# Kernel optimization log

Measured on AMD Instinct MI355X. Metric: run time of the kernel, lower is better.

## Reference

```python
import jax, jax.numpy as jnp
import numpy as np

B, S, E, NUM_CLASSES = 4, 4096, 256, 16

def setup_inputs() -> dict:
    key = jax.random.key(0)
    ks = jax.random.split(key, 10)
    std = E ** -0.5
    return {
        "x":  jax.random.normal(ks[0], (B, S, E), dtype=jnp.float32),
        "wq": jax.random.normal(ks[1], (E, E), dtype=jnp.float32) * std,
        "bq": jnp.zeros((E,), dtype=jnp.float32),
        "wk": jax.random.normal(ks[2], (E, E), dtype=jnp.float32) * std,
        "bk": jnp.zeros((E,), dtype=jnp.float32),
        "wv": jax.random.normal(ks[3], (E, E), dtype=jnp.float32) * std,
        "bv": jnp.zeros((E,), dtype=jnp.float32),
        "wo": jax.random.normal(ks[4], (NUM_CLASSES, E), dtype=jnp.float32) * std,
        "bo": jnp.zeros((NUM_CLASSES,), dtype=jnp.float32),
    }

def reference(x, wq, bq, wk, bk, wv, bv, wo, bo):
    embed_dim = wq.shape[0]
    scaling = embed_dim ** -0.5  # float(embed_dim) ** (-0.5)
    # torch Linear: y = x @ W.T + b
    Q = jnp.einsum('bse,oe->bso', x, wq) + bq
    K = jnp.einsum('bse,oe->bso', x, wk) + bk
    V = jnp.einsum('bse,oe->bso', x, wv) + bv
    # scores: [B, S, S]
    scores = jnp.einsum('bqe,bke->bqk', Q, K) * scaling
    # original code has `/ (embed_dim ^ 0.5)`; intended math is / sqrt(embed_dim)
    attn = jax.nn.softmax(scores, axis=-1) * scaling
    attn_out = jnp.einsum('bqk,bke->bqe', attn, V)
    return jnp.einsum('bqe,oe->bqo', attn_out, wo) + bo
```

## Files before the change

kernel.cpp:

```cpp
#include <hip/hip_runtime.h>
#include <hip/hip_bf16.h>


#define S_ 4096
#define E_ 256
#define B_ 4
#define NC_ 16
#define BS_ (B_ * S_)
#define NS_ 4

typedef __attribute__((ext_vector_type(8))) short bf16x8;
typedef __attribute__((ext_vector_type(4))) float f32x4;

__device__ __forceinline__ unsigned short bf16_rtne(float f) {
    unsigned int u = __float_as_uint(f);
    return (unsigned short)((u + 0x7FFFu + ((u >> 16) & 1u)) >> 16);
}
__device__ __forceinline__ bf16x8 pack8(f32x4 a, f32x4 b) {
    bf16x8 r;
#pragma unroll
    for (int i = 0; i < 4; i++) r[i] = (short)bf16_rtne(a[i]);
#pragma unroll
    for (int i = 0; i < 4; i++) r[4 + i] = (short)bf16_rtne(b[i]);
    return r;
}
__device__ __forceinline__ void gl_lds16(const void* g, void* lds) {
    __builtin_amdgcn_global_load_lds(
        (const __attribute__((address_space(1))) unsigned int*)g,
        (__attribute__((address_space(3))) unsigned int*)lds, 16, 0, 0);
}
__device__ __forceinline__ int swz_u(int q) { return q ^ ((q >> 3) & 7); }

__global__ __launch_bounds__(256) void qkv_gemm(
    const float* __restrict__ x, const float* __restrict__ wq,
    const float* __restrict__ wk, const float* __restrict__ wv,
    const float* __restrict__ bq, const float* __restrict__ bk,
    const float* __restrict__ bv, short* __restrict__ Qb,
    short* __restrict__ Kb, short* __restrict__ Vtc,
    float* __restrict__ partial) {
    __shared__ __align__(16) short stg[2][8192];
    __shared__ __align__(16) short epi[16896];

    int t = threadIdx.x;
    int lin = blockIdx.x;
    int xcd = lin & 7, r8 = lin >> 3;
    int sel = r8 >> 5;
    int m0 = (((xcd << 5) | (r8 & 31))) * 64;
    int lane = t & 63, wid = t >> 6, quad = lane >> 4, idx = lane & 15;

    const float* wsel = (sel == 0) ? wq : (sel == 1) ? wk : wv;
    const float* bias = (sel == 0) ? bq : (sel == 1) ? bk : bv;

    const float* wsrc[4];
#pragma unroll
    for (int i = 0; i < 4; i++) {
        int q = i * 256 + t, u = swz_u(q);
        wsrc[i] = wsel + (size_t)(u >> 2) * E_ + (u & 3) * 8;
    }

    f32x4 wf[8];
#pragma unroll
    for (int i = 0; i < 4; i++) {
        wf[i * 2] = *(const f32x4*)(wsrc[i]);
        wf[i * 2 + 1] = *(const f32x4*)(wsrc[i] + 4);
    }

    {
        int z = lin * 256 + t;
        partial[z] = 0.f;
        if (z < BS_ * NC_ - 196608) partial[z + 196608] = 0.f;
    }

    const float* xrow = x + (size_t)(m0 + wid * 16 + idx) * E_ + quad * 8;
    bf16x8 af[8];
#pragma unroll
    for (int it = 0; it < 8; it++) {
        f32x4 a0 = *(const f32x4*)(xrow + it * 32);
        f32x4 a1 = *(const f32x4*)(xrow + it * 32 + 4);
        af[it] = pack8(a0, a1);
    }

#pragma unroll
    for (int i = 0; i < 4; i++)
        *(bf16x8*)&stg[0][(i * 256 + t) * 8] = pack8(wf[i * 2], wf[i * 2 + 1]);

    f32x4 zf = {0.f, 0.f, 0.f, 0.f};
    f32x4 acc[16];
#pragma unroll
    for (int i = 0; i < 16; i++) acc[i] = zf;

    int fo = (idx * 4 + quad) ^ (idx >> 1);

    __syncthreads();

#pragma unroll
    for (int it = 0; it < 8; it++) {
        if (it < 7) {
            int kc = (it + 1) * 32;
#pragma unroll
            for (int i = 0; i < 4; i++) {
                wf[i * 2] = *(const f32x4*)(wsrc[i] + kc);
                wf[i * 2 + 1] = *(const f32x4*)(wsrc[i] + kc + 4);
            }
        }
        const short* cw = &stg[it & 1][fo * 8];
        __builtin_amdgcn_s_setprio(1);
#pragma unroll
        for (int ct = 0; ct < 16; ct++)
            acc[ct] = __builtin_amdgcn_mfma_f32_16x16x32_bf16(
                af[it], *(const bf16x8*)&cw[ct * 512], acc[ct], 0, 0, 0);
        __builtin_amdgcn_s_setprio(0);
        if (it < 7) {
            short* d = stg[(it + 1) & 1];
#pragma unroll
            for (int i = 0; i < 4; i++)
                *(bf16x8*)&d[(i * 256 + t) * 8] = pack8(wf[i * 2], wf[i * 2 + 1]);
        }
        __syncthreads();
    }

    int qr = quad * 4;
    if (sel == 2) {
#pragma unroll
        for (int ct = 0; ct < 16; ct++) {
            int e = ct * 16 + idx;
            float bb = bias[e];
#pragma unroll
            for (int r = 0; r < 4; r++) {
                int mr = wid * 16 + qr + r;
                int ckg = mr >> 5, sin = mr & 31;
                int sp = ((sin & 15) << 1) | (sin >> 4);
                int pos = (sp >> 3) ^ ((e >> 1) & 3);
                epi[ckg * 8192 + e * 32 + pos * 8 + (sp & 7)] =
                    (short)bf16_rtne(acc[ct][r] + bb);
            }
        }
        __syncthreads();
        size_t base = ((size_t)((m0 >> 12) * 128 + ((m0 & (S_ - 1)) >> 5))) * 8192;
#pragma unroll
        for (int j = 0; j < 8; j++) {
            int unit = j * 256 + t;
            *(bf16x8*)(Vtc + base + (size_t)unit * 8) = *(const bf16x8*)&epi[unit * 8];
        }
    } else {
        float alpha = (sel == 0) ? 0.0625f : 1.0f;
#pragma unroll
        for (int ct = 0; ct < 16; ct++) {
            int n = ct * 16 + idx;
            float bb = bias[n];
#pragma unroll
            for (int r = 0; r < 4; r++) {
                int row = wid * 16 + qr + r;
                int col = (sel == 1) ? ((((n >> 3) ^ (row & 7)) << 3) | (n & 7)) : n;
                epi[row * 264 + col] = (short)bf16_rtne((acc[ct][r] + bb) * alpha);
            }
        }
        __syncthreads();
        short* out = (sel == 0) ? Qb : Kb;
#pragma unroll
        for (int j = 0; j < 8; j++) {
            int g = j * 256 + t;
            int row = g >> 5, seg = g & 31;
            *(bf16x8*)(out + (size_t)(m0 + row) * E_ + seg * 8) =
                *(const bf16x8*)&epi[row * 264 + seg * 8];
        }
    }
}

__global__ __launch_bounds__(256, 2) void flash_attn(
    const short* __restrict__ Qb, const short* __restrict__ Kb,
    const short* __restrict__ Vtc, const float* __restrict__ wo,
    float* __restrict__ partial, float* __restrict__ lpart) {
    __shared__ __align__(16) short lds[37888];

    int t = threadIdx.x;
    int lin = blockIdx.x;
    int xcd = lin & 7, r8 = lin >> 3;
    int pair = (xcd << 1) | (r8 >> 5);
    int b = pair >> 2, slice = pair & 3, q0 = (r8 & 31) * 128;
    int key0 = slice * (S_ / NS_);
    const int nchunk = (S_ / NS_) / 32;
    int lane = t & 63, wv = t >> 6, quad = lane >> 4, idx = lane & 15;

    bf16x8 qf[2][8];
#pragma unroll
    for (int u = 0; u < 2; u++) {
        const short* qrow = Qb + (size_t)(b * S_ + q0 + u * 64 + wv * 16 + idx) * E_ + quad * 8;
#pragma unroll
        for (int c = 0; c < 8; c++) qf[u][c] = *(const bf16x8*)(qrow + c * 32);
    }

    f32x4 zf = {0.f, 0.f, 0.f, 0.f};
    f32x4 oacc[2][16];
#pragma unroll
    for (int u = 0; u < 2; u++)
#pragma unroll
        for (int i = 0; i < 16; i++) oacc[u][i] = zf;
    float ls[2][4] = {{0, 0, 0, 0}, {0, 0, 0, 0}};

    const short* kg = Kb + (size_t)(b * S_ + key0) * E_ + lane * 8;
    const short* vg = Vtc + ((size_t)(b * 128 + (key0 >> 5))) * 8192 + lane * 8;
    short* psw = lds + 32768 + wv * 1280;
    unsigned int* pswu = (unsigned int*)psw;
    int vsw = (quad ^ ((idx >> 1) & 3)) << 3;

#pragma unroll
    for (int j = 0; j < 4; j++) gl_lds16(kg + (wv * 4 + j) * 512, &lds[(wv * 4 + j) * 512]);
#pragma unroll
    for (int j = 0; j < 4; j++) gl_lds16(vg + (wv * 4 + j) * 512, &lds[16384 + (wv * 4 + j) * 512]);
#pragma unroll
    for (int j = 0; j < 4; j++) gl_lds16(kg + 8192 + (wv * 4 + j) * 512, &lds[8192 + (wv * 4 + j) * 512]);
    __syncthreads();

    {
        f32x4 s[4] = {zf, zf, zf, zf};
        __builtin_amdgcn_s_setprio(1);
#pragma unroll
        for (int c = 0; c < 8; c++) {
            int p = (((c * 4 + quad) ^ (idx & 7)) << 3);
            bf16x8 k0 = *(const bf16x8*)&lds[idx * 256 + p];
            bf16x8 k1 = *(const bf16x8*)&lds[(16 + idx) * 256 + p];
            s[0] = __builtin_amdgcn_mfma_f32_16x16x32_bf16(qf[0][c], k0, s[0], 0, 0, 0);
            s[1] = __builtin_amdgcn_mfma_f32_16x16x32_bf16(qf[0][c], k1, s[1], 0, 0, 0);
            s[2] = __builtin_amdgcn_mfma_f32_16x16x32_bf16(qf[1][c], k0, s[2], 0, 0, 0);
            s[3] = __builtin_amdgcn_mfma_f32_16x16x32_bf16(qf[1][c], k1, s[3], 0, 0, 0);
        }
        __builtin_amdgcn_s_setprio(0);
#pragma unroll
        for (int u = 0; u < 2; u++)
#pragma unroll
            for (int r = 0; r < 4; r++) {
                float p0 = __expf(s[u * 2][r]);
                float p1 = __expf(s[u * 2 + 1][r]);
                ls[u][r] += p0 + p1;
                pswu[u * 320 + (quad * 4 + r) * 20 + idx] =
                    (unsigned int)bf16_rtne(p0) | ((unsigned int)bf16_rtne(p1) << 16);
            }
    }

    for (int ck = 0; ck < nchunk - 1; ck++) {
        __syncthreads();
        bf16x8 af0 = *(const bf16x8*)&psw[idx * 40 + quad * 8];
        bf16x8 af1 = *(const bf16x8*)&psw[640 + idx * 40 + quad * 8];
        if (ck + 2 < nchunk) {
            const short* ks = kg + (size_t)(ck + 2) * 8192;
            short* kd = lds + (ck & 1) * 8192;
#pragma unroll
            for (int j = 0; j < 4; j++) gl_lds16(ks + (wv * 4 + j) * 512, &kd[(wv * 4 + j) * 512]);
        }
        {
            const short* vs = vg + (size_t)(ck + 1) * 8192;
            short* vd = lds + 16384 + ((ck + 1) & 1) * 8192;
#pragma unroll
            for (int j = 0; j < 4; j++) gl_lds16(vs + (wv * 4 + j) * 512, &vd[(wv * 4 + j) * 512]);
        }
        const short* kc = lds + ((ck + 1) & 1) * 8192;
        f32x4 s[4] = {zf, zf, zf, zf};
        __builtin_amdgcn_s_setprio(1);
#pragma unroll
        for (int c = 0; c < 8; c++) {
            int p = (((c * 4 + quad) ^ (idx & 7)) << 3);
            bf16x8 k0 = *(const bf16x8*)&kc[idx * 256 + p];
            bf16x8 k1 = *(const bf16x8*)&kc[(16 + idx) * 256 + p];
            s[0] = __builtin_amdgcn_mfma_f32_16x16x32_bf16(qf[0][c], k0, s[0], 0, 0, 0);
            s[1] = __builtin_amdgcn_mfma_f32_16x16x32_bf16(qf[0][c], k1, s[1], 0, 0, 0);
            s[2] = __builtin_amdgcn_mfma_f32_16x16x32_bf16(qf[1][c], k0, s[2], 0, 0, 0);
            s[3] = __builtin_amdgcn_mfma_f32_16x16x32_bf16(qf[1][c], k1, s[3], 0, 0, 0);
        }
        __builtin_amdgcn_s_setprio(0);
#pragma unroll
        for (int u = 0; u < 2; u++)
#pragma unroll
            for (int r = 0; r < 4; r++) {
                float p0 = __expf(s[u * 2][r]);
                float p1 = __expf(s[u * 2 + 1][r]);
                ls[u][r] += p0 + p1;
                pswu[u * 320 + (quad * 4 + r) * 20 + idx] =
                    (unsigned int)bf16_rtne(p0) | ((unsigned int)bf16_rtne(p1) << 16);
            }
        const short* vc = lds + 16384 + (ck & 1) * 8192;
        __builtin_amdgcn_s_setprio(1);
#pragma unroll
        for (int ct = 0; ct < 16; ct++) {
            bf16x8 v = *(const bf16x8*)&vc[(ct * 16 + idx) * 32 + vsw];
            oacc[0][ct] = __builtin_amdgcn_mfma_f32_16x16x32_bf16(af0, v, oacc[0][ct], 0, 0, 0);
            oacc[1][ct] = __builtin_amdgcn_mfma_f32_16x16x32_bf16(af1, v, oacc[1][ct], 0, 0, 0);
        }
        __builtin_amdgcn_s_setprio(0);
    }
    __syncthreads();
    {
        bf16x8 af0 = *(const bf16x8*)&psw[idx * 40 + quad * 8];
        bf16x8 af1 = *(const bf16x8*)&psw[640 + idx * 40 + quad * 8];
        const short* vc = lds + 16384 + ((nchunk - 1) & 1) * 8192;
        __builtin_amdgcn_s_setprio(1);
#pragma unroll
        for (int ct = 0; ct < 16; ct++) {
            bf16x8 v = *(const bf16x8*)&vc[(ct * 16 + idx) * 32 + vsw];
            oacc[0][ct] = __builtin_amdgcn_mfma_f32_16x16x32_bf16(af0, v, oacc[0][ct], 0, 0, 0);
            oacc[1][ct] = __builtin_amdgcn_mfma_f32_16x16x32_bf16(af1, v, oacc[1][ct], 0, 0, 0);
        }
        __builtin_amdgcn_s_setprio(0);
    }
    __syncthreads();

#pragma unroll
    for (int u = 0; u < 2; u++)
#pragma unroll
        for (int r = 0; r < 4; r++) {
            float v = ls[u][r];
            v += __shfl_xor(v, 1);
            v += __shfl_xor(v, 2);
            v += __shfl_xor(v, 4);
            v += __shfl_xor(v, 8);
            if (idx == 0)
                lpart[(size_t)slice * BS_ + b * S_ + q0 + u * 64 + wv * 16 + quad * 4 + r] = v;
        }

    short* scr = lds + wv * 8192;
#pragma unroll
    for (int u = 0; u < 2; u++)
#pragma unroll
        for (int ct = 0; ct < 16; ct++) {
            int e = ct * 16 + idx;
#pragma unroll
            for (int r = 0; r < 4; r++) {
                int lr = quad * 4 + r;
                scr[u * 4096 + lr * 256 + ((((e >> 3) ^ (lr & 7)) << 3) | (e & 7))] =
                    (short)bf16_rtne(oacc[u][ct][r]);
            }
        }

    f32x4 pacc[2] = {zf, zf};
#pragma unroll
    for (int c = 0; c < 8; c++) {
        const float* ws = wo + idx * E_ + c * 32 + quad * 8;
        bf16x8 bw = pack8(*(const f32x4*)ws, *(const f32x4*)(ws + 4));
#pragma unroll
        for (int u = 0; u < 2; u++) {
            bf16x8 pa = *(const bf16x8*)&scr[u * 4096 + idx * 256 +
                                             (((c * 4 + quad) ^ (idx & 7)) << 3)];
            pacc[u] = __builtin_amdgcn_mfma_f32_16x16x32_bf16(pa, bw, pacc[u], 0, 0, 0);
        }
    }
#pragma unroll
    for (int u = 0; u < 2; u++)
#pragma unroll
        for (int r = 0; r < 4; r++) {
            int m = q0 + u * 64 + wv * 16 + quad * 4 + r;
            atomicAdd(&partial[((size_t)b * S_ + m) * NC_ + idx], pacc[u][r]);
        }
}

__global__ __launch_bounds__(256) void norm_out(
    const float* __restrict__ partial, const float* __restrict__ lpart,
    const float* __restrict__ bo, float* __restrict__ out) {
    int t = threadIdx.x;
    int m = blockIdx.x * 16 + (t >> 4), o = t & 15;
    float ltot = 0.f;
#pragma unroll
    for (int ns = 0; ns < NS_; ns++) ltot += lpart[(size_t)ns * BS_ + m];
    size_t i = (size_t)m * NC_ + o;
    out[i] = partial[i] * (0.0625f / ltot) + bo[o];
}

extern "C" void kernel_launch(void* const* d_in, const int* in_sizes, int n_in,
                              void* d_out, int out_size, void* d_ws, size_t ws_size,
                              hipStream_t stream) {
    const float* x  = (const float*)d_in[0];
    const float* wq = (const float*)d_in[1];
    const float* bq = (const float*)d_in[2];
    const float* wk = (const float*)d_in[3];
    const float* bk = (const float*)d_in[4];
    const float* wv = (const float*)d_in[5];
    const float* bv = (const float*)d_in[6];
    const float* wo = (const float*)d_in[7];
    const float* bo = (const float*)d_in[8];
    float* out = (float*)d_out;

    const size_t NEL = (size_t)BS_ * E_;
    short* Qb = (short*)d_ws;
    short* Kb = Qb + NEL;
    short* Vtc = Kb + NEL;
    float* partial = (float*)(Vtc + NEL);
    float* lpart = partial + (size_t)BS_ * NC_;

    qkv_gemm<<<dim3(768), 256, 0, stream>>>(x, wq, wk, wv, bq, bk, bv, Qb, Kb, Vtc, partial);
    flash_attn<<<dim3(512), 256, 0, stream>>>(Qb, Kb, Vtc, wo, partial, lpart);
    norm_out<<<dim3(BS_ / 16), 256, 0, stream>>>(partial, lpart, bo, out);
}
```

Before: 172.6 us.

## Fuse QKV GEMM, attention, and normalization into one persistent kernel with grid barriers

Merges the three kernels into one launch of 512 blocks. The 768 QKV tiles are spread over two passes, and software grid-wide barriers built on atomic counters separate the QKV, attention and output-normalization phases. This removes two kernel launch gaps and the separate norm kernel. In exchange it adds a hipMemsetAsync for the barrier counters, atomic spin-wait barriers, and a tail where only half the blocks run the second QKV pass. It also relies on all 512 blocks being co-resident (2 per CU), or the barrier deadlocks.

```diff
diff --git a/kernel.cpp b/kernel.cpp
--- a/kernel.cpp
+++ b/kernel.cpp
@@ -31,337 +31,342 @@
 }
 __device__ __forceinline__ int swz_u(int q) { return q ^ ((q >> 3) & 7); }
 
-__global__ __launch_bounds__(256) void qkv_gemm(
+__device__ __forceinline__ void gbar(unsigned* ctr, unsigned nblk) {
+    __threadfence();
+    __syncthreads();
+    if (threadIdx.x == 0) {
+        atomicAdd(ctr, 1u);
+        while (atomicAdd(ctr, 0u) < nblk) __builtin_amdgcn_s_sleep(2);
+    }
+    __syncthreads();
+    __threadfence();
+}
+
+__global__ __launch_bounds__(256, 2) void fused(
     const float* __restrict__ x, const float* __restrict__ wq,
     const float* __restrict__ wk, const float* __restrict__ wv,
     const float* __restrict__ bq, const float* __restrict__ bk,
-    const float* __restrict__ bv, short* __restrict__ Qb,
+    const float* __restrict__ bv, const float* __restrict__ wo,
+    const float* __restrict__ bo, short* __restrict__ Qb,
     short* __restrict__ Kb, short* __restrict__ Vtc,
-    float* __restrict__ partial) {
-    __shared__ __align__(16) short stg[2][8192];
-    __shared__ __align__(16) short epi[16896];
-
+    float* __restrict__ partial, float* __restrict__ lpart,
+    unsigned* __restrict__ bars, float* __restrict__ out) {
+    __shared__ __align__(16) short lds[37888];
     int t = threadIdx.x;
-    int lin = blockIdx.x;
-    int xcd = lin & 7, r8 = lin >> 3;
-    int sel = r8 >> 5;
-    int m0 = (((xcd << 5) | (r8 & 31))) * 64;
+    int bid = blockIdx.x;
     int lane = t & 63, wid = t >> 6, quad = lane >> 4, idx = lane & 15;
-
-    const float* wsel = (sel == 0) ? wq : (sel == 1) ? wk : wv;
-    const float* bias = (sel == 0) ? bq : (sel == 1) ? bk : bv;
-
-    const float* wsrc[4];
-#pragma unroll
-    for (int i = 0; i < 4; i++) {
-        int q = i * 256 + t, u = swz_u(q);
-        wsrc[i] = wsel + (size_t)(u >> 2) * E_ + (u & 3) * 8;
-    }
-
-    f32x4 wf[8];
-#pragma unroll
-    for (int i = 0; i < 4; i++) {
-        wf[i * 2] = *(const f32x4*)(wsrc[i]);
-        wf[i * 2 + 1] = *(const f32x4*)(wsrc[i] + 4);
-    }
+    f32x4 zf = {0.f, 0.f, 0.f, 0.f};
 
     {
-        int z = lin * 256 + t;
+        int z = bid * 256 + t;
         partial[z] = 0.f;
-        if (z < BS_ * NC_ - 196608) partial[z + 196608] = 0.f;
-    }
-
-    const float* xrow = x + (size_t)(m0 + wid * 16 + idx) * E_ + quad * 8;
-    bf16x8 af[8];
-#pragma unroll
-    for (int it = 0; it < 8; it++) {
-        f32x4 a0 = *(const f32x4*)(xrow + it * 32);
-        f32x4 a1 = *(const f32x4*)(xrow + it * 32 + 4);
-        af[it] = pack8(a0, a1);
-    }
-
-#pragma unroll
-    for (int i = 0; i < 4; i++)
-        *(bf16x8*)&stg[0][(i * 256 + t) * 8] = pack8(wf[i * 2], wf[i * 2 + 1]);
-
-    f32x4 zf = {0.f, 0.f, 0.f, 0.f};
-    f32x4 acc[16];
-#pragma unroll
-    for (int i = 0; i < 16; i++) acc[i] = zf;
-
-    int fo = (idx * 4 + quad) ^ (idx >> 1);
-
-    __syncthreads();
-
-#pragma unroll
-    for (int it = 0; it < 8; it++) {
-        if (it < 7) {
-            int kc = (it + 1) * 32;
-#pragma unroll
-            for (int i = 0; i < 4; i++) {
-                wf[i * 2] = *(const f32x4*)(wsrc[i] + kc);
-                wf[i * 2 + 1] = *(const f32x4*)(wsrc[i] + kc + 4);
-            }
-        }
-        const short* cw = &stg[it & 1][fo * 8];
-        __builtin_amdgcn_s_setprio(1);
-#pragma unroll
-        for (int ct = 0; ct < 16; ct++)
-            acc[ct] = __builtin_amdgcn_mfma_f32_16x16x32_bf16(
-                af[it], *(const bf16x8*)&cw[ct * 512], acc[ct], 0, 0, 0);
-        __builtin_amdgcn_s_setprio(0);
-        if (it < 7) {
-            short* d = stg[(it + 1) & 1];
-#pragma unroll
-            for (int i = 0; i < 4; i++)
-                *(bf16x8*)&d[(i * 256 + t) * 8] = pack8(wf[i * 2], wf[i * 2 + 1]);
-        }
-        __syncthreads();
-    }
-
-    int qr = quad * 4;
-    if (sel == 2) {
-#pragma unroll
-        for (int ct = 0; ct < 16; ct++) {
-            int e = ct * 16 + idx;
-            float bb = bias[e];
+        partial[z + 131072] = 0.f;
+    }
+    for (int pass = 0; pass < 2; ++pass) {
+        if (pass == 1 && bid >= 256) break;
+        int lin = bid + pass * 512;
+        int xcd = lin & 7, r8 = lin >> 3;
+        int sel = r8 >> 5;
+        int m0 = (((xcd << 5) | (r8 & 31))) * 64;
+
+        const float* wsel = (sel == 0) ? wq : (sel == 1) ? wk : wv;
+        const float* bias = (sel == 0) ? bq : (sel == 1) ? bk : bv;
+        short* ep = lds + 16384;
+
+        const float* wsrc[4];
+#pragma unroll
+        for (int i = 0; i < 4; i++) {
+            int q = i * 256 + t, u = swz_u(q);
+            wsrc[i] = wsel + (size_t)(u >> 2) * E_ + (u & 3) * 8;
+        }
+        f32x4 wf[8];
+#pragma unroll
+        for (int i = 0; i < 4; i++) {
+            wf[i * 2] = *(const f32x4*)(wsrc[i]);
+            wf[i * 2 + 1] = *(const f32x4*)(wsrc[i] + 4);
+        }
+        const float* xrow = x + (size_t)(m0 + wid * 16 + idx) * E_ + quad * 8;
+        bf16x8 af[8];
+#pragma unroll
+        for (int it = 0; it < 8; it++) {
+            f32x4 a0 = *(const f32x4*)(xrow + it * 32);
+            f32x4 a1 = *(const f32x4*)(xrow + it * 32 + 4);
+            af[it] = pack8(a0, a1);
+        }
+#pragma unroll
+        for (int i = 0; i < 4; i++)
+            *(bf16x8*)&lds[(i * 256 + t) * 8] = pack8(wf[i * 2], wf[i * 2 + 1]);
+
+        f32x4 acc[16];
+#pragma unroll
+        for (int i = 0; i < 16; i++) acc[i] = zf;
+        int fo = (idx * 4 + quad) ^ (idx >> 1);
+
+        __syncthreads();
+#pragma unroll
+        for (int it = 0; it < 8; it++) {
+            if (it < 7) {
+                int kc = (it + 1) * 32;
+#pragma unroll
+                for (int i = 0; i < 4; i++) {
+                    wf[i * 2] = *(const f32x4*)(wsrc[i] + kc);
+                    wf[i * 2 + 1] = *(const f32x4*)(wsrc[i] + kc + 4);
+                }
+            }
+            const short* cw = &lds[((it & 1) * 1024 + fo) * 8];
+            __builtin_amdgcn_s_setprio(1);
+#pragma unroll
+            for (int ct = 0; ct < 16; ct++)
+                acc[ct] = __builtin_amdgcn_mfma_f32_16x16x32_bf16(
+                    af[it], *(const bf16x8*)&cw[ct * 512], acc[ct], 0, 0, 0);
+            __builtin_amdgcn_s_setprio(0);
+            if (it < 7) {
+                short* d = lds + ((it + 1) & 1) * 8192;
+#pragma unroll
+                for (int i = 0; i < 4; i++)
+                    *(bf16x8*)&d[(i * 256 + t) * 8] = pack8(wf[i * 2], wf[i * 2 + 1]);
+            }
+            __syncthreads();
+        }
+
+        int qr = quad * 4;
+        if (sel == 2) {
+#pragma unroll
+            for (int ct = 0; ct < 16; ct++) {
+                int e = ct * 16 + idx;
+                float bb = bias[e];
+#pragma unroll
+                for (int r = 0; r < 4; r++) {
+                    int mr = wid * 16 + qr + r;
+                    int ckg = mr >> 5, sin = mr & 31;
+                    int sp = ((sin & 15) << 1) | (sin >> 4);
+                    int pos = (sp >> 3) ^ ((e >> 1) & 3);
+                    ep[ckg * 8192 + e * 32 + pos * 8 + (sp & 7)] =
+                        (short)bf16_rtne(acc[ct][r] + bb);
+                }
+            }
+            __syncthreads();
+            size_t base = ((size_t)((m0 >> 12) * 128 + ((m0 & (S_ - 1)) >> 5))) * 8192;
+#pragma unroll
+            for (int j = 0; j < 8; j++) {
+                int unit = j * 256 + t;
+                *(bf16x8*)(Vtc + base + (size_t)unit * 8) = *(const bf16x8*)&ep[unit * 8];
+            }
+        } else {
+            float alpha = (sel == 0) ? 0.0625f : 1.0f;
+#pragma unroll
+            for (int ct = 0; ct < 16; ct++) {
+                int n = ct * 16 + idx;
+                float bb = bias[n];
+#pragma unroll
+                for (int r = 0; r < 4; r++) {
+                    int row = wid * 16 + qr + r;
+                    int col = (sel == 1) ? ((((n >> 3) ^ (row & 7)) << 3) | (n & 7)) : n;
+                    ep[row * 264 + col] = (short)bf16_rtne((acc[ct][r] + bb) * alpha);
+                }
+            }
+            __syncthreads();
+            short* o = (sel == 0) ? Qb : Kb;
+#pragma unroll
+            for (int j = 0; j < 8; j++) {
+                int g = j * 256 + t;
+                int row = g >> 5, seg = g & 31;
+                *(bf16x8*)(o + (size_t)(m0 + row) * E_ + seg * 8) =
+                    *(const bf16x8*)&ep[row * 264 + seg * 8];
+            }
+        }
+        __syncthreads();
+    }
+
+    gbar(&bars[0], 512);
+
+    {
+        int lin = bid;
+        int xcd = lin & 7, r8 = lin >> 3;
+        int pair = (xcd << 1) | (r8 >> 5);
+        int b = pair >> 2, slice = pair & 3, q0 = (r8 & 31) * 128;
+        int key0 = slice * (S_ / NS_);
+        const int nchunk = (S_ / NS_) / 32;
+        int wv = wid;
+
+        bf16x8 qf[2][8];
+#pragma unroll
+        for (int u = 0; u < 2; u++) {
+            const short* qrow = Qb + (size_t)(b * S_ + q0 + u * 64 + wv * 16 + idx) * E_ + quad * 8;
+#pragma unroll
+            for (int c = 0; c < 8; c++) qf[u][c] = *(const bf16x8*)(qrow + c * 32);
+        }
+        f32x4 oacc[2][16];
+#pragma unroll
+        for (int u = 0; u < 2; u++)
+#pragma unroll
+            for (int i = 0; i < 16; i++) oacc[u][i] = zf;
+        float ls[2][4] = {{0, 0, 0, 0}, {0, 0, 0, 0}};
+
+        const short* kg = Kb + (size_t)(b * S_ + key0) * E_ + lane * 8;
+        const short* vg = Vtc + ((size_t)(b * 128 + (key0 >> 5))) * 8192 + lane * 8;
+        short* psw = lds + 32768 + wv * 1280;
+        unsigned int* pswu = (unsigned int*)psw;
+        int vsw = (quad ^ ((idx >> 1) & 3)) << 3;
+
+#pragma unroll
+        for (int j = 0; j < 4; j++) gl_lds16(kg + (wv * 4 + j) * 512, &lds[(wv * 4 + j) * 512]);
+#pragma unroll
+        for (int j = 0; j < 4; j++) gl_lds16(vg + (wv * 4 + j) * 512, &lds[16384 + (wv * 4 + j) * 512]);
+#pragma unroll
+        for (int j = 0; j < 4; j++) gl_lds16(kg + 8192 + (wv * 4 + j) * 512, &lds[8192 + (wv * 4 + j) * 512]);
+        __syncthreads();
+
+        {
+            f32x4 s[4] = {zf, zf, zf, zf};
+            __builtin_amdgcn_s_setprio(1);
+#pragma unroll
+            for (int c = 0; c < 8; c++) {
+                int p = (((c * 4 + quad) ^ (idx & 7)) << 3);
+                bf16x8 k0 = *(const bf16x8*)&lds[idx * 256 + p];
+                bf16x8 k1 = *(const bf16x8*)&lds[(16 + idx) * 256 + p];
+                s[0] = __builtin_amdgcn_mfma_f32_16x16x32_bf16(qf[0][c], k0, s[0], 0, 0, 0);
+                s[1] = __builtin_amdgcn_mfma_f32_16x16x32_bf16(qf[0][c], k1, s[1], 0, 0, 0);
+                s[2] = __builtin_amdgcn_mfma_f32_16x16x32_bf16(qf[1][c], k0, s[2], 0, 0, 0);
+                s[3] = __builtin_amdgcn_mfma_f32_16x16x32_bf16(qf[1][c], k1, s[3], 0, 0, 0);
+            }
+            __builtin_amdgcn_s_setprio(0);
+#pragma unroll
+            for (int u = 0; u < 2; u++)
+#pragma unroll
+                for (int r = 0; r < 4; r++) {
+                    float p0 = __expf(s[u * 2][r]);
+                    float p1 = __expf(s[u * 2 + 1][r]);
+                    ls[u][r] += p0 + p1;
+                    pswu[u * 320 + (quad * 4 + r) * 20 + idx] =
+                        (unsigned int)bf16_rtne(p0) | ((unsigned int)bf16_rtne(p1) << 16);
+                }
+        }
+
+        for (int ck = 0; ck < nchunk - 1; ck++) {
+            __syncthreads();
+            bf16x8 af0 = *(const bf16x8*)&psw[idx * 40 + quad * 8];
+            bf16x8 af1 = *(const bf16x8*)&psw[640 + idx * 40 + quad * 8];
+            if (ck + 2 < nchunk) {
+                const short* ks = kg + (size_t)(ck + 2) * 8192;
+                short* kd = lds + (ck & 1) * 8192;
+#pragma unroll
+                for (int j = 0; j < 4; j++) gl_lds16(ks + (wv * 4 + j) * 512, &kd[(wv * 4 + j) * 512]);
+            }
+            {
+                const short* vs = vg + (size_t)(ck + 1) * 8192;
+                short* vd = lds + 16384 + ((ck + 1) & 1) * 8192;
+#pragma unroll
+                for (int j = 0; j < 4; j++) gl_lds16(vs + (wv * 4 + j) * 512, &vd[(wv * 4 + j) * 512]);
+            }
+            const short* kc = lds + ((ck + 1) & 1) * 8192;
+            f32x4 s[4] = {zf, zf, zf, zf};
+            __builtin_amdgcn_s_setprio(1);
+#pragma unroll
+            for (int c = 0; c < 8; c++) {
+                int p = (((c * 4 + quad) ^ (idx & 7)) << 3);
+                bf16x8 k0 = *(const bf16x8*)&kc[idx * 256 + p];
+                bf16x8 k1 = *(const bf16x8*)&kc[(16 + idx) * 256 + p];
+                s[0] = __builtin_amdgcn_mfma_f32_16x16x32_bf16(qf[0][c], k0, s[0], 0, 0, 0);
+                s[1] = __builtin_amdgcn_mfma_f32_16x16x32_bf16(qf[0][c], k1, s[1], 0, 0, 0);
+                s[2] = __builtin_amdgcn_mfma_f32_16x16x32_bf16(qf[1][c], k0, s[2], 0, 0, 0);
+                s[3] = __builtin_amdgcn_mfma_f32_16x16x32_bf16(qf[1][c], k1, s[3], 0, 0, 0);
+            }
+            __builtin_amdgcn_s_setprio(0);
+#pragma unroll
+            for (int u = 0; u < 2; u++)
+#pragma unroll
+                for (int r = 0; r < 4; r++) {
+                    float p0 = __expf(s[u * 2][r]);
+                    float p1 = __expf(s[u * 2 + 1][r]);
+                    ls[u][r] += p0 + p1;
+                    pswu[u * 320 + (quad * 4 + r) * 20 + idx] =
+                        (unsigned int)bf16_rtne(p0) | ((unsigned int)bf16_rtne(p1) << 16);
+                }
+            const short* vc = lds + 16384 + (ck & 1) * 8192;
+            __builtin_amdgcn_s_setprio(1);
+#pragma unroll
+            for (int ct = 0; ct < 16; ct++) {
+                bf16x8 v = *(const bf16x8*)&vc[(ct * 16 + idx) * 32 + vsw];
+                oacc[0][ct] = __builtin_amdgcn_mfma_f32_16x16x32_bf16(af0, v, oacc[0][ct], 0, 0, 0);
+                oacc[1][ct] = __builtin_amdgcn_mfma_f32_16x16x32_bf16(af1, v, oacc[1][ct], 0, 0, 0);
+            }
+            __builtin_amdgcn_s_setprio(0);
+        }
+        __syncthreads();
+        {
+            bf16x8 af0 = *(const bf16x8*)&psw[idx * 40 + quad * 8];
+            bf16x8 af1 = *(const bf16x8*)&psw[640 + idx * 40 + quad * 8];
+            const short* vc = lds + 16384 + ((nchunk - 1) & 1) * 8192;
+            __builtin_amdgcn_s_setprio(1);
+#pragma unroll
+            for (int ct = 0; ct < 16; ct++) {
+                bf16x8 v = *(const bf16x8*)&vc[(ct * 16 + idx) * 32 + vsw];
+                oacc[0][ct] = __builtin_amdgcn_mfma_f32_16x16x32_bf16(af0, v, oacc[0][ct], 0, 0, 0);
+                oacc[1][ct] = __builtin_amdgcn_mfma_f32_16x16x32_bf16(af1, v, oacc[1][ct], 0, 0, 0);
+            }
+            __builtin_amdgcn_s_setprio(0);
+        }
+        __syncthreads();
+
+#pragma unroll
+        for (int u = 0; u < 2; u++)
 #pragma unroll
             for (int r = 0; r < 4; r++) {
-                int mr = wid * 16 + qr + r;
-                int ckg = mr >> 5, sin = mr & 31;
-                int sp = ((sin & 15) << 1) | (sin >> 4);
-                int pos = (sp >> 3) ^ ((e >> 1) & 3);
-                epi[ckg * 8192 + e * 32 + pos * 8 + (sp & 7)] =
-                    (short)bf16_rtne(acc[ct][r] + bb);
-            }
-        }
-        __syncthreads();
-        size_t base = ((size_t)((m0 >> 12) * 128 + ((m0 & (S_ - 1)) >> 5))) * 8192;
-#pragma unroll
-        for (int j = 0; j < 8; j++) {
-            int unit = j * 256 + t;
-            *(bf16x8*)(Vtc + base + (size_t)unit * 8) = *(const bf16x8*)&epi[unit * 8];
-        }
-    } else {
-        float alpha = (sel == 0) ? 0.0625f : 1.0f;
-#pragma unroll
-        for (int ct = 0; ct < 16; ct++) {
-            int n = ct * 16 + idx;
-            float bb = bias[n];
+                float v = ls[u][r];
+                v += __shfl_xor(v, 1);
+                v += __shfl_xor(v, 2);
+                v += __shfl_xor(v, 4);
+                v += __shfl_xor(v, 8);
+                if (idx == 0)
+                    lpart[(size_t)slice * BS_ + b * S_ + q0 + u * 64 + wv * 16 + quad * 4 + r] = v;
+            }
+
+        short* scr = lds + wv * 8192;
+#pragma unroll
+        for (int u = 0; u < 2; u++)
+#pragma unroll
+            for (int ct = 0; ct < 16; ct++) {
+                int e = ct * 16 + idx;
+#pragma unroll
+                for (int r = 0; r < 4; r++) {
+                    int lr = quad * 4 + r;
+                    scr[u * 4096 + lr * 256 + ((((e >> 3) ^ (lr & 7)) << 3) | (e & 7))] =
+                        (short)bf16_rtne(oacc[u][ct][r]);
+                }
+            }
+        f32x4 pacc[2] = {zf, zf};
+#pragma unroll
+        for (int c = 0; c < 8; c++) {
+            const float* ws = wo + idx * E_ + c * 32 + quad * 8;
+            bf16x8 bw = pack8(*(const f32x4*)ws, *(const f32x4*)(ws + 4));
+#pragma unroll
+            for (int u = 0; u < 2; u++) {
+                bf16x8 pa = *(const bf16x8*)&scr[u * 4096 + idx * 256 +
+                                                 (((c * 4 + quad) ^ (idx & 7)) << 3)];
+                pacc[u] = __builtin_amdgcn_mfma_f32_16x16x32_bf16(pa, bw, pacc[u], 0, 0, 0);
+            }
+        }
+#pragma unroll
+        for (int u = 0; u < 2; u++)
 #pragma unroll
             for (int r = 0; r < 4; r++) {
-                int row = wid * 16 + qr + r;
-                int col = (sel == 1) ? ((((n >> 3) ^ (row & 7)) << 3) | (n & 7)) : n;
-                epi[row * 264 + col] = (short)bf16_rtne((acc[ct][r] + bb) * alpha);
-            }
-        }
-        __syncthreads();
-        short* out = (sel == 0) ? Qb : Kb;
-#pragma unroll
-        for (int j = 0; j < 8; j++) {
-            int g = j * 256 + t;
-            int row = g >> 5, seg = g & 31;
-            *(bf16x8*)(out + (size_t)(m0 + row) * E_ + seg * 8) =
-                *(const bf16x8*)&epi[row * 264 + seg * 8];
-        }
-    }
-}
-
-__global__ __launch_bounds__(256, 2) void flash_attn(
-    const short* __restrict__ Qb, const short* __restrict__ Kb,
-    const short* __restrict__ Vtc, const float* __restrict__ wo,
-    float* __restrict__ partial, float* __restrict__ lpart) {
-    __shared__ __align__(16) short lds[37888];
-
-    int t = threadIdx.x;
-    int lin = blockIdx.x;
-    int xcd = lin & 7, r8 = lin >> 3;
-    int pair = (xcd << 1) | (r8 >> 5);
-    int b = pair >> 2, slice = pair & 3, q0 = (r8 & 31) * 128;
-    int key0 = slice * (S_ / NS_);
-    const int nchunk = (S_ / NS_) / 32;
-    int lane = t & 63, wv = t >> 6, quad = lane >> 4, idx = lane & 15;
-
-    bf16x8 qf[2][8];
-#pragma unroll
-    for (int u = 0; u < 2; u++) {
-        const short* qrow = Qb + (size_t)(b * S_ + q0 + u * 64 + wv * 16 + idx) * E_ + quad * 8;
-#pragma unroll
-        for (int c = 0; c < 8; c++) qf[u][c] = *(const bf16x8*)(qrow + c * 32);
-    }
-
-    f32x4 zf = {0.f, 0.f, 0.f, 0.f};
-    f32x4 oacc[2][16];
-#pragma unroll
-    for (int u = 0; u < 2; u++)
-#pragma unroll
-        for (int i = 0; i < 16; i++) oacc[u][i] = zf;
-    float ls[2][4] = {{0, 0, 0, 0}, {0, 0, 0, 0}};
-
-    const short* kg = Kb + (size_t)(b * S_ + key0) * E_ + lane * 8;
-    const short* vg = Vtc + ((size_t)(b * 128 + (key0 >> 5))) * 8192 + lane * 8;
-    short* psw = lds + 32768 + wv * 1280;
-    unsigned int* pswu = (unsigned int*)psw;
-    int vsw = (quad ^ ((idx >> 1) & 3)) << 3;
-
-#pragma unroll
-    for (int j = 0; j < 4; j++) gl_lds16(kg + (wv * 4 + j) * 512, &lds[(wv * 4 + j) * 512]);
-#pragma unroll
-    for (int j = 0; j < 4; j++) gl_lds16(vg + (wv * 4 + j) * 512, &lds[16384 + (wv * 4 + j) * 512]);
-#pragma unroll
-    for (int j = 0; j < 4; j++) gl_lds16(kg + 8192 + (wv * 4 + j) * 512, &lds[8192 + (wv * 4 + j) * 512]);
-    __syncthreads();
-
-    {
-        f32x4 s[4] = {zf, zf, zf, zf};
-        __builtin_amdgcn_s_setprio(1);
-#pragma unroll
-        for (int c = 0; c < 8; c++) {
-            int p = (((c * 4 + quad) ^ (idx & 7)) << 3);
-            bf16x8 k0 = *(const bf16x8*)&lds[idx * 256 + p];
-            bf16x8 k1 = *(const bf16x8*)&lds[(16 + idx) * 256 + p];
-            s[0] = __builtin_amdgcn_mfma_f32_16x16x32_bf16(qf[0][c], k0, s[0], 0, 0, 0);
-            s[1] = __builtin_amdgcn_mfma_f32_16x16x32_bf16(qf[0][c], k1, s[1], 0, 0, 0);
-            s[2] = __builtin_amdgcn_mfma_f32_16x16x32_bf16(qf[1][c], k0, s[2], 0, 0, 0);
-            s[3] = __builtin_amdgcn_mfma_f32_16x16x32_bf16(qf[1][c], k1, s[3], 0, 0, 0);
-        }
-        __builtin_amdgcn_s_setprio(0);
-#pragma unroll
-        for (int u = 0; u < 2; u++)
-#pragma unroll
-            for (int r = 0; r < 4; r++) {
-                float p0 = __expf(s[u * 2][r]);
-                float p1 = __expf(s[u * 2 + 1][r]);
-                ls[u][r] += p0 + p1;
-                pswu[u * 320 + (quad * 4 + r) * 20 + idx] =
-                    (unsigned int)bf16_rtne(p0) | ((unsigned int)bf16_rtne(p1) << 16);
-            }
-    }
-
-    for (int ck = 0; ck < nchunk - 1; ck++) {
-        __syncthreads();
-        bf16x8 af0 = *(const bf16x8*)&psw[idx * 40 + quad * 8];
-        bf16x8 af1 = *(const bf16x8*)&psw[640 + idx * 40 + quad * 8];
-        if (ck + 2 < nchunk) {
-            const short* ks = kg + (size_t)(ck + 2) * 8192;
-            short* kd = lds + (ck & 1) * 8192;
-#pragma unroll
-            for (int j = 0; j < 4; j++) gl_lds16(ks + (wv * 4 + j) * 512, &kd[(wv * 4 + j) * 512]);
-        }
-        {
-            const short* vs = vg + (size_t)(ck + 1) * 8192;
-            short* vd = lds + 16384 + ((ck + 1) & 1) * 8192;
-#pragma unroll
-            for (int j = 0; j < 4; j++) gl_lds16(vs + (wv * 4 + j) * 512, &vd[(wv * 4 + j) * 512]);
-        }
-        const short* kc = lds + ((ck + 1) & 1) * 8192;
-        f32x4 s[4] = {zf, zf, zf, zf};
-        __builtin_amdgcn_s_setprio(1);
-#pragma unroll
-        for (int c = 0; c < 8; c++) {
-            int p = (((c * 4 + quad) ^ (idx & 7)) << 3);
-            bf16x8 k0 = *(const bf16x8*)&kc[idx * 256 + p];
-            bf16x8 k1 = *(const bf16x8*)&kc[(16 + idx) * 256 + p];
-            s[0] = __builtin_amdgcn_mfma_f32_16x16x32_bf16(qf[0][c], k0, s[0], 0, 0, 0);
-            s[1] = __builtin_amdgcn_mfma_f32_16x16x32_bf16(qf[0][c], k1, s[1], 0, 0, 0);
-            s[2] = __builtin_amdgcn_mfma_f32_16x16x32_bf16(qf[1][c], k0, s[2], 0, 0, 0);
-            s[3] = __builtin_amdgcn_mfma_f32_16x16x32_bf16(qf[1][c], k1, s[3], 0, 0, 0);
-        }
-        __builtin_amdgcn_s_setprio(0);
-#pragma unroll
-        for (int u = 0; u < 2; u++)
-#pragma unroll
-            for (int r = 0; r < 4; r++) {
-                float p0 = __expf(s[u * 2][r]);
-                float p1 = __expf(s[u * 2 + 1][r]);
-                ls[u][r] += p0 + p1;
-                pswu[u * 320 + (quad * 4 + r) * 20 + idx] =
-                    (unsigned int)bf16_rtne(p0) | ((unsigned int)bf16_rtne(p1) << 16);
-            }
-        const short* vc = lds + 16384 + (ck & 1) * 8192;
-        __builtin_amdgcn_s_setprio(1);
-#pragma unroll
-        for (int ct = 0; ct < 16; ct++) {
-            bf16x8 v = *(const bf16x8*)&vc[(ct * 16 + idx) * 32 + vsw];
-            oacc[0][ct] = __builtin_amdgcn_mfma_f32_16x16x32_bf16(af0, v, oacc[0][ct], 0, 0, 0);
-            oacc[1][ct] = __builtin_amdgcn_mfma_f32_16x16x32_bf16(af1, v, oacc[1][ct], 0, 0, 0);
-        }
-        __builtin_amdgcn_s_setprio(0);
-    }
-    __syncthreads();
-    {
-        bf16x8 af0 = *(const bf16x8*)&psw[idx * 40 + quad * 8];
-        bf16x8 af1 = *(const bf16x8*)&psw[640 + idx * 40 + quad * 8];
-        const short* vc = lds + 16384 + ((nchunk - 1) & 1) * 8192;
-        __builtin_amdgcn_s_setprio(1);
-#pragma unroll
-        for (int ct = 0; ct < 16; ct++) {
-            bf16x8 v = *(const bf16x8*)&vc[(ct * 16 + idx) * 32 + vsw];
-            oacc[0][ct] = __builtin_amdgcn_mfma_f32_16x16x32_bf16(af0, v, oacc[0][ct], 0, 0, 0);
-            oacc[1][ct] = __builtin_amdgcn_mfma_f32_16x16x32_bf16(af1, v, oacc[1][ct], 0, 0, 0);
-        }
-        __builtin_amdgcn_s_setprio(0);
-    }
-    __syncthreads();
-
-#pragma unroll
-    for (int u = 0; u < 2; u++)
-#pragma unroll
-        for (int r = 0; r < 4; r++) {
-            float v = ls[u][r];
-            v += __shfl_xor(v, 1);
-            v += __shfl_xor(v, 2);
-            v += __shfl_xor(v, 4);
-            v += __shfl_xor(v, 8);
-            if (idx == 0)
-                lpart[(size_t)slice * BS_ + b * S_ + q0 + u * 64 + wv * 16 + quad * 4 + r] = v;
-        }
-
-    short* scr = lds + wv * 8192;
-#pragma unroll
-    for (int u = 0; u < 2; u++)
-#pragma unroll
-        for (int ct = 0; ct < 16; ct++) {
-            int e = ct * 16 + idx;
-#pragma unroll
-            for (int r = 0; r < 4; r++) {
-                int lr = quad * 4 + r;
-                scr[u * 4096 + lr * 256 + ((((e >> 3) ^ (lr & 7)) << 3) | (e & 7))] =
-                    (short)bf16_rtne(oacc[u][ct][r]);
-            }
-        }
-
-    f32x4 pacc[2] = {zf, zf};
-#pragma unroll
-    for (int c = 0; c < 8; c++) {
-        const float* ws = wo + idx * E_ + c * 32 + quad * 8;
-        bf16x8 bw = pack8(*(const f32x4*)ws, *(const f32x4*)(ws + 4));
-#pragma unroll
-        for (int u = 0; u < 2; u++) {
-            bf16x8 pa = *(const bf16x8*)&scr[u * 4096 + idx * 256 +
-                                             (((c * 4 + quad) ^ (idx & 7)) << 3)];
-            pacc[u] = __builtin_amdgcn_mfma_f32_16x16x32_bf16(pa, bw, pacc[u], 0, 0, 0);
-        }
-    }
-#pragma unroll
-    for (int u = 0; u < 2; u++)
-#pragma unroll
-        for (int r = 0; r < 4; r++) {
-            int m = q0 + u * 64 + wv * 16 + quad * 4 + r;
-            atomicAdd(&partial[((size_t)b * S_ + m) * NC_ + idx], pacc[u][r]);
-        }
-}
-
-__global__ __launch_bounds__(256) void norm_out(
-    const float* __restrict__ partial, const float* __restrict__ lpart,
-    const float* __restrict__ bo, float* __restrict__ out) {
-    int t = threadIdx.x;
-    int m = blockIdx.x * 16 + (t >> 4), o = t & 15;
-    float ltot = 0.f;
-#pragma unroll
-    for (int ns = 0; ns < NS_; ns++) ltot += lpart[(size_t)ns * BS_ + m];
-    size_t i = (size_t)m * NC_ + o;
-    out[i] = partial[i] * (0.0625f / ltot) + bo[o];
+                int m = q0 + u * 64 + wv * 16 + quad * 4 + r;
+                atomicAdd(&partial[((size_t)b * S_ + m) * NC_ + idx], pacc[u][r]);
+            }
+    }
+
+    gbar(&bars[1], 512);
+
+#pragma unroll
+    for (int k = 0; k < 2; k++) {
+        int e = bid * 512 + k * 256 + t;
+        int m = e >> 4, o = e & 15;
+        float ltot = 0.f;
+#pragma unroll
+        for (int ns = 0; ns < NS_; ns++) ltot += lpart[(size_t)ns * BS_ + m];
+        out[e] = partial[e] * (0.0625f / ltot) + bo[o];
+    }
 }
 
 extern "C" void kernel_launch(void* const* d_in, const int* in_sizes, int n_in,
@@ -384,8 +389,9 @@
     short* Vtc = Kb + NEL;
     float* partial = (float*)(Vtc + NEL);
     float* lpart = partial + (size_t)BS_ * NC_;
-
-    qkv_gemm<<<dim3(768), 256, 0, stream>>>(x, wq, wk, wv, bq, bk, bv, Qb, Kb, Vtc, partial);
-    flash_attn<<<dim3(512), 256, 0, stream>>>(Qb, Kb, Vtc, wo, partial, lpart);
-    norm_out<<<dim3(BS_ / 16), 256, 0, stream>>>(partial, lpart, bo, out);
-}
+    unsigned* bars = (unsigned*)(lpart + (size_t)NS_ * BS_);
+
+    hipMemsetAsync(bars, 0, 2 * sizeof(unsigned), stream);
+    fused<<<dim3(512), 256, 0, stream>>>(x, wq, wk, wv, bq, bk, bv, wo, bo,
+                                         Qb, Kb, Vtc, partial, lpart, bars, out);
+}
```

New measurement: 418.1 us. 2.42x slower.
